# Performance work log

Measured on AMD Instinct MI355X. Metric: run time of the kernel, lower is better.

Reference implementation:

```python
import jax, jax.numpy as jnp
import numpy as np

N, E = 50000, 400000
EMB, IN, HID, HEADS = 128, 128, 128, 3
RRELU_SLOPE = (1.0 / 8.0 + 1.0 / 3.0) / 2.0  # torch.rrelu eval-mode slope


def _gat_conv(h_in, src, dst, W, a_src, a_dst, b, concat):
    """PyG-style GATConv. h_in: [N, F_in]; src/dst: [E'] (self-loops included)."""
    n = h_in.shape[0]
    h = (h_in @ W).reshape(n, HEADS, -1)            # [N, H, C]
    e_src = jnp.sum(h * a_src, axis=-1)             # [N, H]
    e_dst = jnp.sum(h * a_dst, axis=-1)             # [N, H]
    e = jax.nn.leaky_relu(e_src[src] + e_dst[dst], 0.2)  # [E', H]
    # softmax over incoming edges of each target node
    m = jax.ops.segment_max(e, dst, num_segments=n)
    ex = jnp.exp(e - m[dst])
    denom = jax.ops.segment_sum(ex, dst, num_segments=n)
    alpha = ex / denom[dst]                          # [E', H]
    out = jax.ops.segment_sum(h[src] * alpha[:, :, None], dst, num_segments=n)  # [N,H,C]
    out = out.reshape(n, -1) if concat else out.mean(axis=1)
    return out + b


def _rrelu(x):
    return jnp.where(x >= 0, x, x * RRELU_SLOPE)


def setup_inputs() -> dict:
    key = jax.random.key(0)
    ks = jax.random.split(key, 16)
    d_in = IN + EMB

    def glorot(k, shape):
        fan = sum(shape)
        return jax.random.normal(k, shape, jnp.float32) * np.sqrt(2.0 / fan)

    return {
        "z": jax.random.normal(ks[0], (N, EMB), jnp.float32),
        "x": jax.random.normal(ks[1], (N, IN), jnp.float32),
        "ei": jax.random.randint(ks[2], (2, E), 0, N, jnp.int32),
        "W1": glorot(ks[3], (d_in, HEADS * HID)),
        "a1_src": glorot(ks[4], (HEADS, HID)),
        "a1_dst": glorot(ks[5], (HEADS, HID)),
        "b1": jnp.zeros((HID,), jnp.float32),                 # concat=False -> size C
        "W2": glorot(ks[6], (HID, HEADS * HID)),
        "a2_src": glorot(ks[7], (HEADS, HID)),
        "a2_dst": glorot(ks[8], (HEADS, HID)),
        "b2": jnp.zeros((HEADS * HID,), jnp.float32),         # concat=True -> size H*C
        "W_lin": glorot(ks[9], (HEADS * HID, 1)),
        "b_lin": jnp.zeros((1,), jnp.float32),
    }


def reference(z, x, ei, W1, a1_src, a1_dst, b1, W2, a2_src, a2_dst, b2, W_lin, b_lin):
    n = x.shape[0]
    loops = jnp.arange(n, dtype=ei.dtype)
    src = jnp.concatenate([ei[0], loops])  # PyG add_self_loops=True
    dst = jnp.concatenate([ei[1], loops])
    h = jnp.concatenate([z, x], axis=1)
    h = _rrelu(_gat_conv(h, src, dst, W1, a1_src, a1_dst, b1, concat=False))
    h = _rrelu(_gat_conv(h, src, dst, W2, a2_src, a2_dst, b2, concat=True))
    return jax.nn.sigmoid(h @ W_lin + b_lin)
```

## Files before the change

### kernel.cpp

```cpp
#include <hip/hip_runtime.h>
#include <stdint.h>

#define HEADS 3
#define HID 128
#define FDIM (HEADS * HID)

typedef __attribute__((ext_vector_type(8))) short bf16x8;
typedef __attribute__((ext_vector_type(4))) float f32x4;

__device__ __forceinline__ float lrelu(float x) { return x >= 0.f ? x : 0.2f * x; }
__device__ __forceinline__ float rrelu(float x) {
    const float SLOPE = (1.0f / 8.0f + 1.0f / 3.0f) * 0.5f;
    return x >= 0.f ? x : SLOPE * x;
}
__device__ __forceinline__ unsigned short f2bf(float f) {
    union { float f; unsigned u; } c; c.f = f;
    unsigned r = c.u + 0x7FFF + ((c.u >> 16) & 1);
    return (unsigned short)(r >> 16);
}
__device__ __forceinline__ float bf2f(unsigned short b) {
    union { unsigned u; float f; } c; c.u = (unsigned)b << 16;
    return c.f;
}
__device__ __forceinline__ float bflo(unsigned u) {
    union { unsigned u; float f; } c; c.u = u << 16; return c.f;
}
__device__ __forceinline__ float bfhi(unsigned u) {
    union { unsigned u; float f; } c; c.u = u & 0xffff0000u; return c.f;
}

__device__ __forceinline__ void gload_lds16(const void* g, void* l) {
    __builtin_amdgcn_global_load_lds(
        (const __attribute__((address_space(1))) void*)g,
        (__attribute__((address_space(3))) void*)l, 16, 0, 0);
}


__global__ void k_hist(const int* __restrict__ dst, int E, int* __restrict__ cnt) {
    for (int i = blockIdx.x * blockDim.x + threadIdx.x; i < E; i += gridDim.x * blockDim.x)
        atomicAdd(&cnt[dst[i]], 1);
}

#define SC_T 256
#define SC_E 8
#define SC_CHUNK (SC_T * SC_E)

__global__ __launch_bounds__(SC_T) void k_scan1(const int* __restrict__ cnt,
                                                int* __restrict__ exc,
                                                int* __restrict__ bsum, int n) {
    __shared__ int sm[SC_T];
    int b = blockIdx.x, t = threadIdx.x;
    int base = b * SC_CHUNK + t * SC_E;
    int v[SC_E];
    int s = 0;
#pragma unroll
    for (int i = 0; i < SC_E; i++) {
        int idx = base + i;
        v[i] = (idx < n) ? cnt[idx] : 0;
        s += v[i];
    }
    sm[t] = s;
    __syncthreads();
    for (int off = 1; off < SC_T; off <<= 1) {
        int x = (t >= off) ? sm[t - off] : 0;
        __syncthreads();
        sm[t] += x;
        __syncthreads();
    }
    int run = sm[t] - s;
    if (t == SC_T - 1) bsum[b] = sm[t];
#pragma unroll
    for (int i = 0; i < SC_E; i++) {
        int idx = base + i;
        if (idx < n) exc[idx] = run;
        run += v[i];
    }
}

__global__ __launch_bounds__(256) void k_scan2(const int* __restrict__ bsum,
                                               int* __restrict__ bpre, int nb) {
    __shared__ int sm[256];
    int t = threadIdx.x;
    int v = (t < nb) ? bsum[t] : 0;
    sm[t] = v;
    __syncthreads();
    for (int off = 1; off < 256; off <<= 1) {
        int x = (t >= off) ? sm[t - off] : 0;
        __syncthreads();
        sm[t] += x;
        __syncthreads();
    }
    if (t < nb) bpre[t + 1] = sm[t];
    if (t == 0) bpre[0] = 0;
}

__global__ void k_scan3(int* __restrict__ offs, const int* __restrict__ bpre,
                        int* __restrict__ cursor, int n, int nb) {
    int i = blockIdx.x * blockDim.x + threadIdx.x;
    if (i < n) {
        int o = offs[i] + bpre[i / SC_CHUNK];
        offs[i] = o;
        cursor[i] = o;
    }
    if (i == 0) offs[n] = bpre[nb];
}

__global__ void k_scatter(const int* __restrict__ src, const int* __restrict__ dst, int E,
                          int* __restrict__ cursor, int* __restrict__ ssrc,
                          int* __restrict__ sdst) {
    for (int i = blockIdx.x * blockDim.x + threadIdx.x; i < E; i += gridDim.x * blockDim.x) {
        int d = dst[i];
        int p = atomicAdd(&cursor[d], 1);
        ssrc[p] = src[i];
        sdst[p] = d;
    }
}


__global__ void k_cvt_concat(const float* __restrict__ z, const float* __restrict__ x,
                             unsigned short* __restrict__ A, int Nn, int Mpad) {
    int total = Mpad * 64;
    for (int i = blockIdx.x * blockDim.x + threadIdx.x; i < total;
         i += gridDim.x * blockDim.x) {
        int row = i >> 6;
        int c4 = (i & 63) * 4;
        float4 v = make_float4(0.f, 0.f, 0.f, 0.f);
        if (row < Nn) {
            const float* sp = (c4 < 128) ? (z + (size_t)row * 128 + c4)
                                         : (x + (size_t)row * 128 + (c4 - 128));
            v = *(const float4*)sp;
        }
        unsigned short o[4] = {f2bf(v.x), f2bf(v.y), f2bf(v.z), f2bf(v.w)};
        *(uint2*)&A[(size_t)row * 256 + c4] = *(uint2*)o;
    }
}

__global__ void k_cvt_wt(const float* __restrict__ W, unsigned short* __restrict__ WT,
                         int K, int Ncols) {
    int n = blockIdx.x;
    for (int k = threadIdx.x; k < K; k += blockDim.x)
        WT[(size_t)n * K + k] = f2bf(W[(size_t)k * Ncols + n]);
}


__global__ __launch_bounds__(256) void k_gemm_bf16(
    const unsigned short* __restrict__ A,
    const unsigned short* __restrict__ BT,
    unsigned short* __restrict__ C,
    int K, int Ncols) {
    __shared__ __align__(16) unsigned short As[128 * 32];
    __shared__ __align__(16) unsigned short Bs[128 * 32];
    int tid = threadIdx.x;
    int w = tid >> 6, lane = tid & 63;
    int row0 = blockIdx.x * 128;
    int col0 = blockIdx.y * 128;
    int wr = w >> 1, wc = w & 1;

    f32x4 acc[4][4] = {};
    int frow = lane & 15;
    int fk = (lane >> 4) * 8;

    for (int k0 = 0; k0 < K; k0 += 32) {
#pragma unroll
        for (int i = 0; i < 2; i++) {
            int c = (i * 4 + w) * 64 + lane;
            gload_lds16(A + (size_t)(row0 + (c >> 2)) * K + k0 + (c & 3) * 8,
                        (char*)As + (i * 4 + w) * 1024);
        }
#pragma unroll
        for (int i = 0; i < 2; i++) {
            int c = (i * 4 + w) * 64 + lane;
            gload_lds16(BT + (size_t)(col0 + (c >> 2)) * K + k0 + (c & 3) * 8,
                        (char*)Bs + (i * 4 + w) * 1024);
        }
        asm volatile("s_waitcnt vmcnt(0)" ::: "memory");
        __syncthreads();

        bf16x8 af[4], bfr[4];
#pragma unroll
        for (int m = 0; m < 4; m++)
            af[m] = *(const bf16x8*)&As[(wr * 64 + m * 16 + frow) * 32 + fk];
#pragma unroll
        for (int n = 0; n < 4; n++)
            bfr[n] = *(const bf16x8*)&Bs[(wc * 64 + n * 16 + frow) * 32 + fk];
#pragma unroll
        for (int m = 0; m < 4; m++)
#pragma unroll
            for (int n = 0; n < 4; n++)
                acc[m][n] = __builtin_amdgcn_mfma_f32_16x16x32_bf16(af[m], bfr[n], acc[m][n], 0, 0, 0);
        __syncthreads();
    }

    int ccol = lane & 15, crow = (lane >> 4) * 4;
#pragma unroll
    for (int m = 0; m < 4; m++)
#pragma unroll
        for (int n = 0; n < 4; n++)
#pragma unroll
            for (int j = 0; j < 4; j++) {
                int r = row0 + wr * 64 + m * 16 + crow + j;
                int cc = col0 + wc * 64 + n * 16 + ccol;
                C[(size_t)r * Ncols + cc] = f2bf(acc[m][n][j]);
            }
}


__global__ __launch_bounds__(192) void k_edge_logits(const unsigned short* __restrict__ H,
                                                     const float* __restrict__ asrc,
                                                     const float* __restrict__ adst,
                                                     float* __restrict__ es,
                                                     float* __restrict__ ed, int Nn) {
    int n = blockIdx.x;
    int t = threadIdx.x;
    int h = t >> 6, q = t & 63;
    int col = h * HID + 2 * q;
    unsigned u = *(const unsigned*)&H[(size_t)n * FDIM + col];
    float2 av = *(const float2*)&asrc[col];
    float2 dv = *(const float2*)&adst[col];
    float v0 = bflo(u), v1 = bfhi(u);
    float ps = v0 * av.x + v1 * av.y;
    float pd = v0 * dv.x + v1 * dv.y;
#pragma unroll
    for (int off = 32; off > 0; off >>= 1) {
        ps += __shfl_down(ps, off);
        pd += __shfl_down(pd, off);
    }
    if (q == 0) {
        es[n * HEADS + h] = ps;
        ed[n * HEADS + h] = pd;
    }
}


__global__ void k_edge_w(const int* __restrict__ ssrc, const int* __restrict__ sdst,
                         const float* __restrict__ es, const float* __restrict__ ed,
                         float4* __restrict__ w4, int E) {
    for (int j = blockIdx.x * blockDim.x + threadIdx.x; j < E; j += gridDim.x * blockDim.x) {
        int s = ssrc[j], d = sdst[j];
        float w0 = __expf(lrelu(es[s * 3 + 0] + ed[d * 3 + 0]));
        float w1 = __expf(lrelu(es[s * 3 + 1] + ed[d * 3 + 1]));
        float w2 = __expf(lrelu(es[s * 3 + 2] + ed[d * 3 + 2]));
        w4[j] = make_float4(w0, w1, w2, 0.f);
    }
}

__global__ void k_den(const float* __restrict__ es, const float* __restrict__ ed,
                      const int* __restrict__ offs, const float4* __restrict__ w4,
                      float4* __restrict__ wself, float4* __restrict__ invden, int Nn) {
    for (int n = blockIdx.x * blockDim.x + threadIdx.x; n < Nn; n += gridDim.x * blockDim.x) {
        float s0 = __expf(lrelu(es[n * 3 + 0] + ed[n * 3 + 0]));
        float s1 = __expf(lrelu(es[n * 3 + 1] + ed[n * 3 + 1]));
        float s2 = __expf(lrelu(es[n * 3 + 2] + ed[n * 3 + 2]));
        float d0 = s0, d1 = s1, d2 = s2;
        int j0 = offs[n], j1 = offs[n + 1];
        int j = j0;
        for (; j + 4 <= j1; j += 4) {
            float4 a = w4[j], b = w4[j + 1], c = w4[j + 2], d = w4[j + 3];
            d0 += a.x + b.x + c.x + d.x;
            d1 += a.y + b.y + c.y + d.y;
            d2 += a.z + b.z + c.z + d.z;
        }
        for (; j < j1; j++) {
            float4 w = w4[j];
            d0 += w.x; d1 += w.y; d2 += w.z;
        }
        wself[n] = make_float4(s0, s1, s2, 0.f);
        invden[n] = make_float4(1.f / d0, 1.f / d1, 1.f / d2, 0.f);
    }
}


__global__ __launch_bounds__(192) void k_gat_mean(const unsigned short* __restrict__ H,
                                                  const float* __restrict__ w4f,
                                                  const float* __restrict__ wselff,
                                                  const float* __restrict__ invdenf,
                                                  const int* __restrict__ offs,
                                                  const int* __restrict__ ssrc,
                                                  const float* __restrict__ b,
                                                  unsigned short* __restrict__ out, int Nn) {
    int n = blockIdx.x;
    int t = threadIdx.x;
    int h = t >> 6, q = t & 63;
    int cidx = (h * HID + 2 * q) >> 1;
    const unsigned* Hu = (const unsigned*)H;
    unsigned u = Hu[(size_t)n * 192 + cidx];
    float wsh = wselff[n * 4 + h];
    float a0 = wsh * bflo(u), a1 = wsh * bfhi(u);
    int j0 = offs[n], j1 = offs[n + 1];
    int j = j0;
    for (; j + 4 <= j1; j += 4) {
        int s0 = ssrc[j], s1 = ssrc[j + 1], s2 = ssrc[j + 2], s3 = ssrc[j + 3];
        float w0 = w4f[(size_t)j * 4 + h];
        float w1 = w4f[(size_t)(j + 1) * 4 + h];
        float w2 = w4f[(size_t)(j + 2) * 4 + h];
        float w3 = w4f[(size_t)(j + 3) * 4 + h];
        unsigned u0 = Hu[(size_t)s0 * 192 + cidx];
        unsigned u1 = Hu[(size_t)s1 * 192 + cidx];
        unsigned u2 = Hu[(size_t)s2 * 192 + cidx];
        unsigned u3 = Hu[(size_t)s3 * 192 + cidx];
        a0 = fmaf(w0, bflo(u0), a0); a1 = fmaf(w0, bfhi(u0), a1);
        a0 = fmaf(w1, bflo(u1), a0); a1 = fmaf(w1, bfhi(u1), a1);
        a0 = fmaf(w2, bflo(u2), a0); a1 = fmaf(w2, bfhi(u2), a1);
        a0 = fmaf(w3, bflo(u3), a0); a1 = fmaf(w3, bfhi(u3), a1);
    }
    for (; j < j1; j++) {
        int s = ssrc[j];
        float w = w4f[(size_t)j * 4 + h];
        unsigned uu = Hu[(size_t)s * 192 + cidx];
        a0 = fmaf(w, bflo(uu), a0); a1 = fmaf(w, bfhi(uu), a1);
    }
    float iv = invdenf[n * 4 + h];
    a0 *= iv; a1 *= iv;
    __shared__ float sm[3][128];
    sm[h][2 * q] = a0;
    sm[h][2 * q + 1] = a1;
    __syncthreads();
    if (t < 64) {
        int c0 = 2 * t;
        float m0 = (sm[0][c0] + sm[1][c0] + sm[2][c0]) * (1.f / 3.f) + b[c0];
        float m1 = (sm[0][c0 + 1] + sm[1][c0 + 1] + sm[2][c0 + 1]) * (1.f / 3.f) + b[c0 + 1];
        unsigned short o[2] = {f2bf(rrelu(m0)), f2bf(rrelu(m1))};
        *(unsigned*)&out[(size_t)n * HID + c0] = *(unsigned*)o;
    }
}


__global__ __launch_bounds__(192) void k_gat_cat_final(const unsigned short* __restrict__ H,
                                                       const float* __restrict__ w4f,
                                                       const float* __restrict__ wselff,
                                                       const float* __restrict__ invdenf,
                                                       const int* __restrict__ offs,
                                                       const int* __restrict__ ssrc,
                                                       const float* __restrict__ b,
                                                       const float* __restrict__ Wl,
                                                       const float* __restrict__ bl,
                                                       float* __restrict__ out, int Nn) {
    int n = blockIdx.x;
    int t = threadIdx.x;
    int h = t >> 6, q = t & 63;
    int col = h * HID + 2 * q;
    int cidx = col >> 1;
    const unsigned* Hu = (const unsigned*)H;
    unsigned u = Hu[(size_t)n * 192 + cidx];
    float wsh = wselff[n * 4 + h];
    float a0 = wsh * bflo(u), a1 = wsh * bfhi(u);
    int j0 = offs[n], j1 = offs[n + 1];
    int j = j0;
    for (; j + 4 <= j1; j += 4) {
        int s0 = ssrc[j], s1 = ssrc[j + 1], s2 = ssrc[j + 2], s3 = ssrc[j + 3];
        float w0 = w4f[(size_t)j * 4 + h];
        float w1 = w4f[(size_t)(j + 1) * 4 + h];
        float w2 = w4f[(size_t)(j + 2) * 4 + h];
        float w3 = w4f[(size_t)(j + 3) * 4 + h];
        unsigned u0 = Hu[(size_t)s0 * 192 + cidx];
        unsigned u1 = Hu[(size_t)s1 * 192 + cidx];
        unsigned u2 = Hu[(size_t)s2 * 192 + cidx];
        unsigned u3 = Hu[(size_t)s3 * 192 + cidx];
        a0 = fmaf(w0, bflo(u0), a0); a1 = fmaf(w0, bfhi(u0), a1);
        a0 = fmaf(w1, bflo(u1), a0); a1 = fmaf(w1, bfhi(u1), a1);
        a0 = fmaf(w2, bflo(u2), a0); a1 = fmaf(w2, bfhi(u2), a1);
        a0 = fmaf(w3, bflo(u3), a0); a1 = fmaf(w3, bfhi(u3), a1);
    }
    for (; j < j1; j++) {
        int s = ssrc[j];
        float w = w4f[(size_t)j * 4 + h];
        unsigned uu = Hu[(size_t)s * 192 + cidx];
        a0 = fmaf(w, bflo(uu), a0); a1 = fmaf(w, bfhi(uu), a1);
    }
    float iv = invdenf[n * 4 + h];
    float r0 = rrelu(a0 * iv + b[col]);
    float r1 = rrelu(a1 * iv + b[col + 1]);
    float p = r0 * Wl[col] + r1 * Wl[col + 1];
#pragma unroll
    for (int off = 32; off > 0; off >>= 1) p += __shfl_down(p, off);
    __shared__ float red[3];
    if (q == 0) red[h] = p;
    __syncthreads();
    if (t == 0) out[n] = 1.f / (1.f + __expf(-(red[0] + red[1] + red[2] + bl[0])));
}


extern "C" void kernel_launch(void* const* d_in, const int* in_sizes, int n_in,
                              void* d_out, int out_size, void* d_ws, size_t ws_size,
                              hipStream_t stream) {
    const float* z   = (const float*)d_in[0];
    const float* x   = (const float*)d_in[1];
    const int*   ei  = (const int*)d_in[2];
    const float* W1  = (const float*)d_in[3];
    const float* a1s = (const float*)d_in[4];
    const float* a1d = (const float*)d_in[5];
    const float* b1  = (const float*)d_in[6];
    const float* W2  = (const float*)d_in[7];
    const float* a2s = (const float*)d_in[8];
    const float* a2d = (const float*)d_in[9];
    const float* b2  = (const float*)d_in[10];
    const float* Wl  = (const float*)d_in[11];
    const float* bl  = (const float*)d_in[12];
    float* outp = (float*)d_out;

    int Nn = in_sizes[0] / 128;
    int E  = in_sizes[2] / 2;
    int Mpad = (Nn + 127) & ~127;
    int nb = (Nn + SC_CHUNK - 1) / SC_CHUNK;

    char* p = (char*)d_ws;
    auto carve = [&](size_t bytes) -> char* {
        char* r = p;
        p += (bytes + 255) & ~(size_t)255;
        return r;
    };
    int*            offs   = (int*)carve((size_t)(Nn + 1) * 4);
    int*            cursor = (int*)carve((size_t)Nn * 4);
    int*            ssrc   = (int*)carve((size_t)E * 4);
    int*            sdst   = (int*)carve((size_t)E * 4);
    int*            bsum   = (int*)carve((size_t)(nb + 1) * 4);
    int*            bpre   = (int*)carve((size_t)(nb + 1) * 4);
    float*          e1s    = (float*)carve((size_t)Nn * 3 * 4);
    float*          e1d    = (float*)carve((size_t)Nn * 3 * 4);
    float4*         w4     = (float4*)carve((size_t)E * 16);
    float4*         wself  = (float4*)carve((size_t)Nn * 16);
    float4*         invden = (float4*)carve((size_t)Nn * 16);
    unsigned short* Abf    = (unsigned short*)carve((size_t)Mpad * 256 * 2);
    unsigned short* W1T    = (unsigned short*)carve((size_t)FDIM * 256 * 2);
    unsigned short* W2T    = (unsigned short*)carve((size_t)FDIM * 128 * 2);
    unsigned short* Hbf    = (unsigned short*)carve((size_t)Mpad * FDIM * 2);
    unsigned short* H2in   = (unsigned short*)carve((size_t)Mpad * 128 * 2);

    const int* srcI = ei;
    const int* dstI = ei + E;

    hipMemsetAsync(cursor, 0, (size_t)Nn * 4, stream);
    k_hist<<<256, 256, 0, stream>>>(dstI, E, cursor);
    k_scan1<<<nb, SC_T, 0, stream>>>(cursor, offs, bsum, Nn);
    k_scan2<<<1, 256, 0, stream>>>(bsum, bpre, nb);
    k_scan3<<<(Nn + 255) / 256, 256, 0, stream>>>(offs, bpre, cursor, Nn, nb);
    k_scatter<<<256, 256, 0, stream>>>(srcI, dstI, E, cursor, ssrc, sdst);

    k_cvt_concat<<<2048, 256, 0, stream>>>(z, x, Abf, Nn, Mpad);
    k_cvt_wt<<<FDIM, 256, 0, stream>>>(W1, W1T, 256, FDIM);
    k_cvt_wt<<<FDIM, 128, 0, stream>>>(W2, W2T, 128, FDIM);
    hipMemsetAsync(H2in + (size_t)Nn * 128, 0, (size_t)(Mpad - Nn) * 128 * 2, stream);

    dim3 gg(Mpad / 128, FDIM / 128);

    k_gemm_bf16<<<gg, 256, 0, stream>>>(Abf, W1T, Hbf, 256, FDIM);
    k_edge_logits<<<Nn, 192, 0, stream>>>(Hbf, a1s, a1d, e1s, e1d, Nn);
    k_edge_w<<<1024, 256, 0, stream>>>(ssrc, sdst, e1s, e1d, w4, E);
    k_den<<<(Nn + 255) / 256, 256, 0, stream>>>(e1s, e1d, offs, w4, wself, invden, Nn);
    k_gat_mean<<<Nn, 192, 0, stream>>>(Hbf, (const float*)w4, (const float*)wself,
                                       (const float*)invden, offs, ssrc, b1, H2in, Nn);

    k_gemm_bf16<<<gg, 256, 0, stream>>>(H2in, W2T, Hbf, 128, FDIM);
    k_edge_logits<<<Nn, 192, 0, stream>>>(Hbf, a2s, a2d, e1s, e1d, Nn);
    k_edge_w<<<1024, 256, 0, stream>>>(ssrc, sdst, e1s, e1d, w4, E);
    k_den<<<(Nn + 255) / 256, 256, 0, stream>>>(e1s, e1d, offs, w4, wself, invden, Nn);
    k_gat_cat_final<<<Nn, 192, 0, stream>>>(Hbf, (const float*)w4, (const float*)wself,
                                            (const float*)invden, offs, ssrc, b2, Wl, bl,
                                            outp, Nn);
}
```

Baseline: 299.3 us.

## Fuse attention logit computation into GEMM epilogue and unroll aggregation gather by 8

Attention source/destination logits are now computed in the GEMM epilogue from the fp32 accumulators, using cross-lane shuffles and a shared-memory combine across the two column halves, so the separate per-node logit kernel and its re-read of H are gone. The neighbor aggregation loops in both GAT kernels become a shared macro that batches 8 edges at a time, keeping more gather loads in flight. Logits now come from fp32 rather than bf16-rounded H, which changes numerics slightly. The epilogue adds shuffles, a barrier and extra registers to the GEMM.

```diff
diff --git a/kernel.cpp b/kernel.cpp
--- a/kernel.cpp
+++ b/kernel.cpp
@@ -17,10 +17,6 @@
     union { float f; unsigned u; } c; c.f = f;
     unsigned r = c.u + 0x7FFF + ((c.u >> 16) & 1);
     return (unsigned short)(r >> 16);
-}
-__device__ __forceinline__ float bf2f(unsigned short b) {
-    union { unsigned u; float f; } c; c.u = (unsigned)b << 16;
-    return c.f;
 }
 __device__ __forceinline__ float bflo(unsigned u) {
     union { unsigned u; float f; } c; c.u = u << 16; return c.f;
@@ -147,9 +143,12 @@
     const unsigned short* __restrict__ A,
     const unsigned short* __restrict__ BT,
     unsigned short* __restrict__ C,
-    int K, int Ncols) {
+    int K, int Ncols,
+    const float* __restrict__ asrc, const float* __restrict__ adst,
+    float* __restrict__ es, float* __restrict__ ed, int Nnodes) {
     __shared__ __align__(16) unsigned short As[128 * 32];
     __shared__ __align__(16) unsigned short Bs[128 * 32];
+    __shared__ float esP[128][2], edP[128][2];
     int tid = threadIdx.x;
     int w = tid >> 6, lane = tid & 63;
     int row0 = blockIdx.x * 128;
@@ -192,6 +191,7 @@
     }
 
     int ccol = lane & 15, crow = (lane >> 4) * 4;
+
 #pragma unroll
     for (int m = 0; m < 4; m++)
 #pragma unroll
@@ -202,32 +202,44 @@
                 int cc = col0 + wc * 64 + n * 16 + ccol;
                 C[(size_t)r * Ncols + cc] = f2bf(acc[m][n][j]);
             }
-}
-
-
-__global__ __launch_bounds__(192) void k_edge_logits(const unsigned short* __restrict__ H,
-                                                     const float* __restrict__ asrc,
-                                                     const float* __restrict__ adst,
-                                                     float* __restrict__ es,
-                                                     float* __restrict__ ed, int Nn) {
-    int n = blockIdx.x;
-    int t = threadIdx.x;
-    int h = t >> 6, q = t & 63;
-    int col = h * HID + 2 * q;
-    unsigned u = *(const unsigned*)&H[(size_t)n * FDIM + col];
-    float2 av = *(const float2*)&asrc[col];
-    float2 dv = *(const float2*)&adst[col];
-    float v0 = bflo(u), v1 = bfhi(u);
-    float ps = v0 * av.x + v1 * av.y;
-    float pd = v0 * dv.x + v1 * dv.y;
-#pragma unroll
-    for (int off = 32; off > 0; off >>= 1) {
-        ps += __shfl_down(ps, off);
-        pd += __shfl_down(pd, off);
-    }
-    if (q == 0) {
-        es[n * HEADS + h] = ps;
-        ed[n * HEADS + h] = pd;
+
+    int head = blockIdx.y;
+    float as4[4], ad4[4];
+#pragma unroll
+    for (int n = 0; n < 4; n++) {
+        int col_sub = wc * 64 + n * 16 + ccol;
+        as4[n] = asrc[head * HID + col_sub];
+        ad4[n] = adst[head * HID + col_sub];
+    }
+#pragma unroll
+    for (int m = 0; m < 4; m++)
+#pragma unroll
+        for (int j = 0; j < 4; j++) {
+            float ps = 0.f, pd = 0.f;
+#pragma unroll
+            for (int n = 0; n < 4; n++) {
+                float v = acc[m][n][j];
+                ps = fmaf(v, as4[n], ps);
+                pd = fmaf(v, ad4[n], pd);
+            }
+#pragma unroll
+            for (int off = 1; off < 16; off <<= 1) {
+                ps += __shfl_xor(ps, off);
+                pd += __shfl_xor(pd, off);
+            }
+            if (ccol == 0) {
+                int row_sub = wr * 64 + m * 16 + crow + j;
+                esP[row_sub][wc] = ps;
+                edP[row_sub][wc] = pd;
+            }
+        }
+    __syncthreads();
+    if (tid < 128) {
+        int r = row0 + tid;
+        if (r < Nnodes) {
+            es[(size_t)r * 3 + head] = esP[tid][0] + esP[tid][1];
+            ed[(size_t)r * 3 + head] = edP[tid][0] + edP[tid][1];
+        }
     }
 }
 
@@ -269,6 +281,35 @@
     }
 }
 
+
+#define AGG_BODY(acc_update)                                                      \
+    int j = j0;                                                                   \
+    for (; j + 8 <= j1; j += 8) {                                                 \
+        int s[8]; float wv[8]; unsigned uu[8];                                    \
+        _Pragma("unroll") for (int e = 0; e < 8; e++) s[e] = ssrc[j + e];         \
+        _Pragma("unroll") for (int e = 0; e < 8; e++)                             \
+            wv[e] = w4f[(size_t)(j + e) * 4 + h];                                 \
+        _Pragma("unroll") for (int e = 0; e < 8; e++)                             \
+            uu[e] = Hu[(size_t)s[e] * 192 + cidx];                                \
+        _Pragma("unroll") for (int e = 0; e < 8; e++) { acc_update(wv[e], uu[e]) }\
+    }                                                                             \
+    for (; j + 4 <= j1; j += 4) {                                                 \
+        int s[4]; float wv[4]; unsigned uu[4];                                    \
+        _Pragma("unroll") for (int e = 0; e < 4; e++) s[e] = ssrc[j + e];         \
+        _Pragma("unroll") for (int e = 0; e < 4; e++)                             \
+            wv[e] = w4f[(size_t)(j + e) * 4 + h];                                 \
+        _Pragma("unroll") for (int e = 0; e < 4; e++)                             \
+            uu[e] = Hu[(size_t)s[e] * 192 + cidx];                                \
+        _Pragma("unroll") for (int e = 0; e < 4; e++) { acc_update(wv[e], uu[e]) }\
+    }                                                                             \
+    for (; j < j1; j++) {                                                         \
+        int s = ssrc[j];                                                          \
+        float w = w4f[(size_t)j * 4 + h];                                         \
+        unsigned u1 = Hu[(size_t)s * 192 + cidx];                                 \
+        { acc_update(w, u1) }                                                     \
+    }
+
+#define ACC_UPD(wv, uv) a0 = fmaf(wv, bflo(uv), a0); a1 = fmaf(wv, bfhi(uv), a1);
 
 __global__ __launch_bounds__(192) void k_gat_mean(const unsigned short* __restrict__ H,
                                                   const float* __restrict__ w4f,
@@ -287,28 +328,7 @@
     float wsh = wselff[n * 4 + h];
     float a0 = wsh * bflo(u), a1 = wsh * bfhi(u);
     int j0 = offs[n], j1 = offs[n + 1];
-    int j = j0;
-    for (; j + 4 <= j1; j += 4) {
-        int s0 = ssrc[j], s1 = ssrc[j + 1], s2 = ssrc[j + 2], s3 = ssrc[j + 3];
-        float w0 = w4f[(size_t)j * 4 + h];
-        float w1 = w4f[(size_t)(j + 1) * 4 + h];
-        float w2 = w4f[(size_t)(j + 2) * 4 + h];
-        float w3 = w4f[(size_t)(j + 3) * 4 + h];
-        unsigned u0 = Hu[(size_t)s0 * 192 + cidx];
-        unsigned u1 = Hu[(size_t)s1 * 192 + cidx];
-        unsigned u2 = Hu[(size_t)s2 * 192 + cidx];
-        unsigned u3 = Hu[(size_t)s3 * 192 + cidx];
-        a0 = fmaf(w0, bflo(u0), a0); a1 = fmaf(w0, bfhi(u0), a1);
-        a0 = fmaf(w1, bflo(u1), a0); a1 = fmaf(w1, bfhi(u1), a1);
-        a0 = fmaf(w2, bflo(u2), a0); a1 = fmaf(w2, bfhi(u2), a1);
-        a0 = fmaf(w3, bflo(u3), a0); a1 = fmaf(w3, bfhi(u3), a1);
-    }
-    for (; j < j1; j++) {
-        int s = ssrc[j];
-        float w = w4f[(size_t)j * 4 + h];
-        unsigned uu = Hu[(size_t)s * 192 + cidx];
-        a0 = fmaf(w, bflo(uu), a0); a1 = fmaf(w, bfhi(uu), a1);
-    }
+    AGG_BODY(ACC_UPD)
     float iv = invdenf[n * 4 + h];
     a0 *= iv; a1 *= iv;
     __shared__ float sm[3][128];
@@ -345,28 +365,7 @@
     float wsh = wselff[n * 4 + h];
     float a0 = wsh * bflo(u), a1 = wsh * bfhi(u);
     int j0 = offs[n], j1 = offs[n + 1];
-    int j = j0;
-    for (; j + 4 <= j1; j += 4) {
-        int s0 = ssrc[j], s1 = ssrc[j + 1], s2 = ssrc[j + 2], s3 = ssrc[j + 3];
-        float w0 = w4f[(size_t)j * 4 + h];
-        float w1 = w4f[(size_t)(j + 1) * 4 + h];
-        float w2 = w4f[(size_t)(j + 2) * 4 + h];
-        float w3 = w4f[(size_t)(j + 3) * 4 + h];
-        unsigned u0 = Hu[(size_t)s0 * 192 + cidx];
-        unsigned u1 = Hu[(size_t)s1 * 192 + cidx];
-        unsigned u2 = Hu[(size_t)s2 * 192 + cidx];
-        unsigned u3 = Hu[(size_t)s3 * 192 + cidx];
-        a0 = fmaf(w0, bflo(u0), a0); a1 = fmaf(w0, bfhi(u0), a1);
-        a0 = fmaf(w1, bflo(u1), a0); a1 = fmaf(w1, bfhi(u1), a1);
-        a0 = fmaf(w2, bflo(u2), a0); a1 = fmaf(w2, bfhi(u2), a1);
-        a0 = fmaf(w3, bflo(u3), a0); a1 = fmaf(w3, bfhi(u3), a1);
-    }
-    for (; j < j1; j++) {
-        int s = ssrc[j];
-        float w = w4f[(size_t)j * 4 + h];
-        unsigned uu = Hu[(size_t)s * 192 + cidx];
-        a0 = fmaf(w, bflo(uu), a0); a1 = fmaf(w, bfhi(uu), a1);
-    }
+    AGG_BODY(ACC_UPD)
     float iv = invdenf[n * 4 + h];
     float r0 = rrelu(a0 * iv + b[col]);
     float r1 = rrelu(a1 * iv + b[col + 1]);
@@ -443,15 +442,13 @@
 
     dim3 gg(Mpad / 128, FDIM / 128);
 
-    k_gemm_bf16<<<gg, 256, 0, stream>>>(Abf, W1T, Hbf, 256, FDIM);
-    k_edge_logits<<<Nn, 192, 0, stream>>>(Hbf, a1s, a1d, e1s, e1d, Nn);
+    k_gemm_bf16<<<gg, 256, 0, stream>>>(Abf, W1T, Hbf, 256, FDIM, a1s, a1d, e1s, e1d, Nn);
     k_edge_w<<<1024, 256, 0, stream>>>(ssrc, sdst, e1s, e1d, w4, E);
     k_den<<<(Nn + 255) / 256, 256, 0, stream>>>(e1s, e1d, offs, w4, wself, invden, Nn);
     k_gat_mean<<<Nn, 192, 0, stream>>>(Hbf, (const float*)w4, (const float*)wself,
                                        (const float*)invden, offs, ssrc, b1, H2in, Nn);
 
-    k_gemm_bf16<<<gg, 256, 0, stream>>>(H2in, W2T, Hbf, 128, FDIM);
-    k_edge_logits<<<Nn, 192, 0, stream>>>(Hbf, a2s, a2d, e1s, e1d, Nn);
+    k_gemm_bf16<<<gg, 256, 0, stream>>>(H2in, W2T, Hbf, 128, FDIM, a2s, a2d, e1s, e1d, Nn);
     k_edge_w<<<1024, 256, 0, stream>>>(ssrc, sdst, e1s, e1d, w4, E);
     k_den<<<(Nn + 255) / 256, 256, 0, stream>>>(e1s, e1d, offs, w4, wself, invden, Nn);
     k_gat_cat_final<<<Nn, 192, 0, stream>>>(Hbf, (const float*)w4, (const float*)wself,
```

Result: faster. 267.2 us (-10.7%).
